# Optimization experiments

Hardware: AMD Instinct MI355X
Metric: run time of the kernel (lower is better)

The kernel has to match this reference:

```python
import jax, jax.numpy as jnp
import numpy as np

TOKENS, IN_F, OUT_F = 8192, 4096, 4096

def setup_inputs() -> dict:
    key = jax.random.key(0)
    k1, k2, k3, k4 = jax.random.split(key, 4)
    # int8 activations and weights in [-127, 127]
    x = jax.random.randint(k1, (TOKENS, IN_F), -127, 128, dtype=jnp.int32).astype(jnp.int8)
    weight = jax.random.randint(k2, (OUT_F, IN_F), -127, 128, dtype=jnp.int32).astype(jnp.int8)  # [out, in]
    # static per-output-channel dequant scale (fp16), small so fp16 output doesn't overflow
    dequant_scale = (jax.random.uniform(k3, (OUT_F,), dtype=jnp.float32) * 1e-3).astype(jnp.float16)
    bias = (jax.random.normal(k4, (OUT_F,), dtype=jnp.float32)).astype(jnp.float16)
    return {"x": x, "weight": weight, "dequant_scale": dequant_scale, "bias": bias}

def reference(x, weight, dequant_scale, bias):
    # int8 GEMM with int32 accumulation: [tokens, in] @ [in, out] -> [tokens, out]
    acc = jax.lax.dot_general(
        x, weight.T,
        dimension_numbers=(((1,), (0,)), ((), ())),
        preferred_element_type=jnp.int32,
    )
    # static per-output-channel dequant, cast to fp16, add fp16 bias
    out = (acc.astype(jnp.float32) * dequant_scale.astype(jnp.float32)[None, :]).astype(jnp.float16)
    out = out + bias[None, :]
    # module returns (output, output_bias)
    return (out, bias)
```

## Files before the change

### kernel.cpp

```cpp
#include <hip/hip_runtime.h>
#include <hip/hip_fp16.h>
#include <stdint.h>

typedef __attribute__((ext_vector_type(4))) int int32x4;
typedef __attribute__((ext_vector_type(4))) float float32x4;

#define TOKENS 8192
#define IN_F   4096
#define OUT_F  4096
#define BM 256
#define BN 256
#define BK 128
#define NT (IN_F / BK)
#define ESTR 260

#define AS1 __attribute__((address_space(1)))
#define AS3 __attribute__((address_space(3)))

__global__ __launch_bounds__(256)
void pack_all_kernel(const int* __restrict__ x32, const int* __restrict__ w32,
                     const float* __restrict__ bias,
                     uint32_t* __restrict__ x8, uint32_t* __restrict__ w8,
                     float* __restrict__ bias_out)
{
    const int gid = blockIdx.x * 256 + threadIdx.x;
    if (gid < OUT_F / 4) {
        float32x4 b4 = __builtin_nontemporal_load((const float32x4*)bias + gid);
        __builtin_nontemporal_store(b4, (float32x4*)bias_out + gid);
    }

    const int nx4 = TOKENS * IN_F / 4;
    const int nw4 = OUT_F * IN_F / 4;
    for (int i = gid; i < nx4 + nw4; i += gridDim.x * 256) {
        const int* s; uint32_t* d; int j;
        if (i < nx4) { s = x32; d = x8; j = i; }
        else         { s = w32; d = w8; j = i - nx4; }
        int32x4 v = __builtin_nontemporal_load((const int32x4*)s + j);
        d[j] = (uint32_t)(v[0] & 0xff) | ((uint32_t)(v[1] & 0xff) << 8) |
               ((uint32_t)(v[2] & 0xff) << 16) | ((uint32_t)v[3] << 24);
    }
}

__global__ __launch_bounds__(512, 2)
void w8a8_gemm_kernel(const int8_t* __restrict__ x,
                      const int8_t* __restrict__ w,
                      const float* __restrict__ scale,
                      const float* __restrict__ bias,
                      float* __restrict__ out)
{
    __shared__ int8_t smem[131072];
    int8_t* lA = smem;
    int8_t* lB = smem + 65536;

    const int tid = threadIdx.x;
    const int wv  = tid >> 6;
    const int l   = tid & 63;
    const int wqm = wv >> 1;
    const int wqn = wv & 1;

    const int xc  = blockIdx.x & 7;
    const int idx = blockIdx.x >> 3;
    const int bn  = (xc & 1) * 8 + (idx & 7);
    const int bm  = (xc >> 1) * 8 + (idx >> 3);

    const int8_t* baseA = x + (size_t)bm * BM * IN_F;
    const int8_t* baseB = w + (size_t)bn * BN * IN_F;

    const int seg0 = wv * 2, seg1 = wv * 2 + 1;
    const int r8   = l >> 3;
    const int swc  = (((l & 7) ^ r8) << 4);

    const int8_t* pA0 = baseA + (size_t)(seg0 * 8 + r8) * IN_F + swc;
    const int8_t* pA1 = baseA + (size_t)(seg1 * 8 + r8) * IN_F + swc;
    const int8_t* pB0 = baseB + (size_t)(seg0 * 8 + r8) * IN_F + swc;
    const int8_t* pB1 = baseB + (size_t)(seg1 * 8 + r8) * IN_F + swc;

    const int fr  = l & 15;
    const int xk  = (l & 7) << 4;
    const int cb0 = (l >> 4) << 4;

    int32x4 acc[2][2][2][4];
#pragma unroll
    for (int a0 = 0; a0 < 2; ++a0)
#pragma unroll
        for (int a1 = 0; a1 < 2; ++a1)
#pragma unroll
            for (int a2 = 0; a2 < 2; ++a2)
#pragma unroll
                for (int a3 = 0; a3 < 4; ++a3)
                    acc[a0][a1][a2][a3] = (int32x4){0, 0, 0, 0};

    int32x4 aF[2][2][2];
    int32x4 bF[2][4][2];

    auto stage_half = [&](int h4) {
        const int kt_ = h4 >> 2;
        const int wh_ = h4 & 3;
        const size_t off = (size_t)(wh_ & 1) * (128 * IN_F) + (size_t)kt_ * BK;
        const int8_t* s0 = ((wh_ < 2) ? pA0 : pB0) + off;
        const int8_t* s1 = ((wh_ < 2) ? pA1 : pB1) + off;
        int8_t* db = ((wh_ < 2) ? lA : lB) + ((kt_ & 1) << 15) + ((wh_ & 1) << 14);
        __builtin_amdgcn_global_load_lds(
            (const AS1 void*)s0, (AS3 void*)(db + seg0 * 1024), 16, 0, 0);
        __builtin_amdgcn_global_load_lds(
            (const AS1 void*)s1, (AS3 void*)(db + seg1 * 1024), 16, 0, 0);
    };

#define LDA(MH)                                                                        \
    do {                                                                               \
        _Pragma("unroll") for (int mi = 0; mi < 2; ++mi)                               \
        _Pragma("unroll") for (int ks = 0; ks < 2; ++ks)                               \
            aF[MH][mi][ks] = *(const int32x4*)&lAb[((MH) << 14) +                      \
                (wqm * 32 + mi * 16 + fr) * 128 + (((ks * 64) + cb0) ^ xk)];           \
    } while (0)

#define LDB(NH)                                                                        \
    do {                                                                               \
        _Pragma("unroll") for (int ni = 0; ni < 4; ++ni)                               \
        _Pragma("unroll") for (int ks = 0; ks < 2; ++ks)                               \
            bF[NH][ni][ks] = *(const int32x4*)&lBb[((NH) << 14) +                      \
                (wqn * 64 + ni * 16 + fr) * 128 + (((ks * 64) + cb0) ^ xk)];           \
    } while (0)

#define MMAQ(MH, NH)                                                                   \
    do {                                                                               \
        _Pragma("unroll") for (int mi = 0; mi < 2; ++mi)                               \
        _Pragma("unroll") for (int ni = 0; ni < 4; ++ni)                               \
        _Pragma("unroll") for (int ks = 0; ks < 2; ++ks)                               \
            acc[MH][NH][mi][ni] = __builtin_amdgcn_mfma_i32_16x16x64_i8(               \
                aF[MH][mi][ks], bF[NH][ni][ks], acc[MH][NH][mi][ni], 0, 0, 0);         \
    } while (0)

    stage_half(0); stage_half(1); stage_half(2); stage_half(3);
    asm volatile("s_waitcnt vmcnt(0)" ::: "memory");
    __builtin_amdgcn_s_barrier();

    for (int t = 0; t < NT; ++t) {
        const int8_t* lAb = lA + ((t & 1) << 15);
        const int8_t* lBb = lB + ((t & 1) << 15);

        LDA(0); LDB(0); LDB(1); LDA(1);

        if (t + 1 < NT) {
            stage_half(4 * (t + 1) + 0); stage_half(4 * (t + 1) + 1);
            stage_half(4 * (t + 1) + 2); stage_half(4 * (t + 1) + 3);
        }

        __builtin_amdgcn_s_setprio(1);
        MMAQ(0, 0); MMAQ(0, 1); MMAQ(1, 0); MMAQ(1, 1);
        __builtin_amdgcn_s_setprio(0);

        if (t + 1 < NT) asm volatile("s_waitcnt vmcnt(0)" ::: "memory");
        __builtin_amdgcn_s_barrier();
    }

    __syncthreads();
    int* eL = (int*)smem;
    const int c4   = tid & 63;
    const int rowt = tid >> 6;
    const float32x4 sc4 = ((const float32x4*)scale)[bn * 64 + c4];
    const float32x4 bf4 = ((const float32x4*)bias )[bn * 64 + c4];
    const __half bh[4] = { __float2half(bf4[0]), __float2half(bf4[1]),
                           __float2half(bf4[2]), __float2half(bf4[3]) };
    const int r0 = (l >> 4) << 2;
    const int wr0 = (wqm & 1) * 32 + r0;

    for (int c = 0; c < 4; ++c) {
        if ((wqm >> 1) == (c & 1)) {
            const int MH = c >> 1;
#pragma unroll
            for (int NH = 0; NH < 2; ++NH)
#pragma unroll
                for (int mi = 0; mi < 2; ++mi)
#pragma unroll
                    for (int ni = 0; ni < 4; ++ni)
#pragma unroll
                        for (int r = 0; r < 4; ++r)
                            eL[(wr0 + mi * 16 + r) * ESTR +
                               NH * 128 + wqn * 64 + ni * 16 + fr] = acc[MH][NH][mi][ni][r];
        }
        __syncthreads();
#pragma unroll
        for (int p = 0; p < 8; ++p) {
            const int rl = p * 8 + rowt;
            int32x4 v = *(const int32x4*)&eL[rl * ESTR + c4 * 4];
            float32x4 o;
#pragma unroll
            for (int j = 0; j < 4; ++j) {
                __half h = __float2half((float)v[j] * sc4[j]);
                o[j] = __half2float(__hadd(h, bh[j]));
            }
            const size_t rowg = (size_t)(bm * 256 + c * 64 + rl);
            __builtin_nontemporal_store(o, (float32x4*)out + rowg * (OUT_F / 4) + bn * 64 + c4);
        }
        __syncthreads();
    }
#undef LDA
#undef LDB
#undef MMAQ
}

extern "C" void kernel_launch(void* const* d_in, const int* in_sizes, int n_in,
                              void* d_out, int out_size, void* d_ws, size_t ws_size,
                              hipStream_t stream)
{
    const int*   x32   = (const int*)d_in[0];
    const int*   w32   = (const int*)d_in[1];
    const float* scale = (const float*)d_in[2];
    const float* bias  = (const float*)d_in[3];
    float* out = (float*)d_out;

    int8_t* x8 = (int8_t*)d_ws;
    int8_t* w8 = x8 + (size_t)TOKENS * IN_F;

    pack_all_kernel<<<3072, 256, 0, stream>>>(x32, w32, bias, (uint32_t*)x8, (uint32_t*)w8,
                                              out + (size_t)TOKENS * OUT_F);

    w8a8_gemm_kernel<<<512, 512, 0, stream>>>(x8, w8, scale, bias, out);
}
```

Baseline: 185.9 us.

## Double-buffer MFMA fragments across K halves and prefetch global tiles two ahead

The main loop now splits each K tile into two 64-wide halves, each with its own register fragment set. LDS reads for one half are issued while the MFMAs of the other half run, and the first half of the next tile is read before the current tile's second-half MFMAs. Global-to-LDS staging is issued for tile t+2 into the buffer just freed, and the prologue preloads two tiles. The goal is to hide LDS read latency behind matrix math. The cost is an extra barrier and lgkmcnt wait per iteration, plus more fragment registers, which may pressure occupancy at 2 waves per SIMD.

```diff
diff --git a/kernel.cpp b/kernel.cpp
--- a/kernel.cpp
+++ b/kernel.cpp
@@ -81,17 +81,17 @@
 
     int32x4 acc[2][2][2][4];
 #pragma unroll
-    for (int a0 = 0; a0 < 2; ++a0)
-#pragma unroll
-        for (int a1 = 0; a1 < 2; ++a1)
-#pragma unroll
-            for (int a2 = 0; a2 < 2; ++a2)
-#pragma unroll
-                for (int a3 = 0; a3 < 4; ++a3)
-                    acc[a0][a1][a2][a3] = (int32x4){0, 0, 0, 0};
-
-    int32x4 aF[2][2][2];
-    int32x4 bF[2][4][2];
+    for (int a0i = 0; a0i < 2; ++a0i)
+#pragma unroll
+        for (int a1i = 0; a1i < 2; ++a1i)
+#pragma unroll
+            for (int a2i = 0; a2i < 2; ++a2i)
+#pragma unroll
+                for (int a3i = 0; a3i < 4; ++a3i)
+                    acc[a0i][a1i][a2i][a3i] = (int32x4){0, 0, 0, 0};
+
+    int32x4 a0[2][2], b0[2][4];
+    int32x4 a1[2][2], b1[2][4];
 
     auto stage_half = [&](int h4) {
         const int kt_ = h4 >> 2;
@@ -105,52 +105,64 @@
         __builtin_amdgcn_global_load_lds(
             (const AS1 void*)s1, (AS3 void*)(db + seg1 * 1024), 16, 0, 0);
     };
-
-#define LDA(MH)                                                                        \
+    auto stage_tile = [&](int tt) {
+        stage_half(4 * tt + 0); stage_half(4 * tt + 1);
+        stage_half(4 * tt + 2); stage_half(4 * tt + 3);
+    };
+
+#define LDFA(DST, LABP, KS)                                                            \
     do {                                                                               \
+        _Pragma("unroll") for (int MH = 0; MH < 2; ++MH)                               \
         _Pragma("unroll") for (int mi = 0; mi < 2; ++mi)                               \
-        _Pragma("unroll") for (int ks = 0; ks < 2; ++ks)                               \
-            aF[MH][mi][ks] = *(const int32x4*)&lAb[((MH) << 14) +                      \
-                (wqm * 32 + mi * 16 + fr) * 128 + (((ks * 64) + cb0) ^ xk)];           \
+            DST[MH][mi] = *(const int32x4*)&(LABP)[(MH << 14) +                        \
+                (wqm * 32 + mi * 16 + fr) * 128 + ((((KS) * 64) + cb0) ^ xk)];         \
     } while (0)
 
-#define LDB(NH)                                                                        \
+#define LDFB(DST, LBBP, KS)                                                            \
     do {                                                                               \
+        _Pragma("unroll") for (int NH = 0; NH < 2; ++NH)                               \
         _Pragma("unroll") for (int ni = 0; ni < 4; ++ni)                               \
-        _Pragma("unroll") for (int ks = 0; ks < 2; ++ks)                               \
-            bF[NH][ni][ks] = *(const int32x4*)&lBb[((NH) << 14) +                      \
-                (wqn * 64 + ni * 16 + fr) * 128 + (((ks * 64) + cb0) ^ xk)];           \
+            DST[NH][ni] = *(const int32x4*)&(LBBP)[(NH << 14) +                        \
+                (wqn * 64 + ni * 16 + fr) * 128 + ((((KS) * 64) + cb0) ^ xk)];         \
     } while (0)
 
-#define MMAQ(MH, NH)                                                                   \
+#define MMA_ALL(AS_, BS_)                                                              \
     do {                                                                               \
+        _Pragma("unroll") for (int MH = 0; MH < 2; ++MH)                               \
+        _Pragma("unroll") for (int NH = 0; NH < 2; ++NH)                               \
         _Pragma("unroll") for (int mi = 0; mi < 2; ++mi)                               \
         _Pragma("unroll") for (int ni = 0; ni < 4; ++ni)                               \
-        _Pragma("unroll") for (int ks = 0; ks < 2; ++ks)                               \
             acc[MH][NH][mi][ni] = __builtin_amdgcn_mfma_i32_16x16x64_i8(               \
-                aF[MH][mi][ks], bF[NH][ni][ks], acc[MH][NH][mi][ni], 0, 0, 0);         \
+                AS_[MH][mi], BS_[NH][ni], acc[MH][NH][mi][ni], 0, 0, 0);               \
     } while (0)
 
-    stage_half(0); stage_half(1); stage_half(2); stage_half(3);
+    stage_tile(0); stage_tile(1);
     asm volatile("s_waitcnt vmcnt(0)" ::: "memory");
     __builtin_amdgcn_s_barrier();
+    LDFA(a0, lA, 0); LDFB(b0, lB, 0);
 
     for (int t = 0; t < NT; ++t) {
-        const int8_t* lAb = lA + ((t & 1) << 15);
-        const int8_t* lBb = lB + ((t & 1) << 15);
-
-        LDA(0); LDB(0); LDB(1); LDA(1);
-
-        if (t + 1 < NT) {
-            stage_half(4 * (t + 1) + 0); stage_half(4 * (t + 1) + 1);
-            stage_half(4 * (t + 1) + 2); stage_half(4 * (t + 1) + 3);
-        }
-
+        const int8_t* curA = lA + ((t & 1) << 15);
+        const int8_t* curB = lB + ((t & 1) << 15);
+        const int8_t* othA = lA + (((t + 1) & 1) << 15);
+        const int8_t* othB = lB + (((t + 1) & 1) << 15);
+
+        LDFA(a1, curA, 1); LDFB(b1, curB, 1);
         __builtin_amdgcn_s_setprio(1);
-        MMAQ(0, 0); MMAQ(0, 1); MMAQ(1, 0); MMAQ(1, 1);
+        MMA_ALL(a0, b0);
         __builtin_amdgcn_s_setprio(0);
-
-        if (t + 1 < NT) asm volatile("s_waitcnt vmcnt(0)" ::: "memory");
+        __builtin_amdgcn_sched_barrier(0);
+        asm volatile("s_waitcnt lgkmcnt(0)" ::: "memory");
+        __builtin_amdgcn_s_barrier();
+
+        if (t + 1 < NT) { LDFA(a0, othA, 0); LDFB(b0, othB, 0); }
+        if (t + 2 < NT) stage_tile(t + 2);
+        __builtin_amdgcn_s_setprio(1);
+        MMA_ALL(a1, b1);
+        __builtin_amdgcn_s_setprio(0);
+        __builtin_amdgcn_sched_barrier(0);
+        asm volatile("s_waitcnt lgkmcnt(0)" ::: "memory");
+        if (t + 2 < NT) asm volatile("s_waitcnt vmcnt(0)" ::: "memory");
         __builtin_amdgcn_s_barrier();
     }
 
@@ -195,9 +207,9 @@
         }
         __syncthreads();
     }
-#undef LDA
-#undef LDB
-#undef MMAQ
+#undef LDFA
+#undef LDFB
+#undef MMA_ALL
 }
 
 extern "C" void kernel_launch(void* const* d_in, const int* in_sizes, int n_in,
```

Measured after the change: 188.0 us. No clear change (+1.1%).

## Remap warps to 128x64 tiles and software-pipeline LDS reads with MFMA phases

Applied to the files above, without the earlier changes.

Each warp now owns 128 rows (4 chunks of 32) by 64 columns instead of the earlier quadrant-split mapping. The k-tile is split into four phases, and each phase issues the LDS reads for the next A chunk while the current chunk's MFMAs run, using double-buffered A and B fragment registers. Global-to-LDS staging is split so that the B half for tile t+2 is issued early, with partial vmcnt and lgkmcnt waits and barriers between phases. The aim is to hide LDS latency and global load latency behind MFMA work, at the cost of more barriers and a fragile hand-tuned wait-count schedule.

```diff
diff --git a/kernel.cpp b/kernel.cpp
--- a/kernel.cpp
+++ b/kernel.cpp
@@ -55,8 +55,10 @@
     const int tid = threadIdx.x;
     const int wv  = tid >> 6;
     const int l   = tid & 63;
-    const int wqm = wv >> 1;
-    const int wqn = wv & 1;
+    const int mgrp = wv >> 2;
+    const int ncol = wv & 3;
+    const int bhalf = ncol >> 1;
+    const int brow  = (ncol & 1) * 64;
 
     const int xc  = blockIdx.x & 7;
     const int idx = blockIdx.x >> 3;
@@ -79,19 +81,17 @@
     const int xk  = (l & 7) << 4;
     const int cb0 = (l >> 4) << 4;
 
-    int32x4 acc[2][2][2][4];
-#pragma unroll
-    for (int a0 = 0; a0 < 2; ++a0)
-#pragma unroll
-        for (int a1 = 0; a1 < 2; ++a1)
-#pragma unroll
-            for (int a2 = 0; a2 < 2; ++a2)
-#pragma unroll
-                for (int a3 = 0; a3 < 4; ++a3)
-                    acc[a0][a1][a2][a3] = (int32x4){0, 0, 0, 0};
-
-    int32x4 aF[2][2][2];
-    int32x4 bF[2][4][2];
+    int32x4 acc[4][2][4];
+#pragma unroll
+    for (int q = 0; q < 4; ++q)
+#pragma unroll
+        for (int mi = 0; mi < 2; ++mi)
+#pragma unroll
+            for (int ni = 0; ni < 4; ++ni)
+                acc[q][mi][ni] = (int32x4){0, 0, 0, 0};
+
+    int32x4 aE[2][2], aO[2][2];
+    int32x4 bS0[4][2], bS1[4][2];
 
     auto stage_half = [&](int h4) {
         const int kt_ = h4 >> 2;
@@ -106,52 +106,80 @@
             (const AS1 void*)s1, (AS3 void*)(db + seg1 * 1024), 16, 0, 0);
     };
 
-#define LDA(MH)                                                                        \
-    do {                                                                               \
+#define LDCH(DST, TT, Q)                                                               \
+    do {                                                                               \
+        const int8_t* _p = lA + (((TT) & 1) << 15) + (mgrp << 14);                     \
         _Pragma("unroll") for (int mi = 0; mi < 2; ++mi)                               \
         _Pragma("unroll") for (int ks = 0; ks < 2; ++ks)                               \
-            aF[MH][mi][ks] = *(const int32x4*)&lAb[((MH) << 14) +                      \
-                (wqm * 32 + mi * 16 + fr) * 128 + (((ks * 64) + cb0) ^ xk)];           \
-    } while (0)
-
-#define LDB(NH)                                                                        \
-    do {                                                                               \
+            DST[mi][ks] = *(const int32x4*)&_p[((Q) * 32 + mi * 16 + fr) * 128 +       \
+                                               (((ks * 64) + cb0) ^ xk)];              \
+    } while (0)
+
+#define LDBO(DST, TT)                                                                  \
+    do {                                                                               \
+        const int8_t* _p = lB + (((TT) & 1) << 15) + (bhalf << 14);                    \
         _Pragma("unroll") for (int ni = 0; ni < 4; ++ni)                               \
         _Pragma("unroll") for (int ks = 0; ks < 2; ++ks)                               \
-            bF[NH][ni][ks] = *(const int32x4*)&lBb[((NH) << 14) +                      \
-                (wqn * 64 + ni * 16 + fr) * 128 + (((ks * 64) + cb0) ^ xk)];           \
-    } while (0)
-
-#define MMAQ(MH, NH)                                                                   \
+            DST[ni][ks] = *(const int32x4*)&_p[(brow + ni * 16 + fr) * 128 +           \
+                                               (((ks * 64) + cb0) ^ xk)];              \
+    } while (0)
+
+#define MMACH(Q, ASET, BSET)                                                           \
     do {                                                                               \
         _Pragma("unroll") for (int mi = 0; mi < 2; ++mi)                               \
         _Pragma("unroll") for (int ni = 0; ni < 4; ++ni)                               \
         _Pragma("unroll") for (int ks = 0; ks < 2; ++ks)                               \
-            acc[MH][NH][mi][ni] = __builtin_amdgcn_mfma_i32_16x16x64_i8(               \
-                aF[MH][mi][ks], bF[NH][ni][ks], acc[MH][NH][mi][ni], 0, 0, 0);         \
+            acc[Q][mi][ni] = __builtin_amdgcn_mfma_i32_16x16x64_i8(                    \
+                ASET[mi][ks], BSET[ni][ks], acc[Q][mi][ni], 0, 0, 0);                  \
+    } while (0)
+
+#define PH_TAIL(Q, ASET, BCUR)                                                         \
+        __builtin_amdgcn_sched_barrier(0);                                             \
+        __builtin_amdgcn_s_setprio(1);                                                 \
+        MMACH(Q, ASET, BCUR);                                                          \
+        __builtin_amdgcn_s_setprio(0);                                                 \
+        __builtin_amdgcn_s_barrier()
+
+#define TILE(T, BCUR, BNXT)                                                            \
+    do {                                                                               \
+                      \
+        LDCH(aO, T, 1);                                                                \
+        if ((T) + 1 < NT) { stage_half(4 * ((T) + 1) + 0);                             \
+                            stage_half(4 * ((T) + 1) + 1); }                           \
+        __builtin_amdgcn_s_barrier();                                                  \
+        asm volatile("s_waitcnt lgkmcnt(4)" ::: "memory");                             \
+        PH_TAIL(0, aE, BCUR);                                                          \
+                                                    \
+        LDCH(aE, T, 2);                                                                \
+        __builtin_amdgcn_s_barrier();                                                  \
+        asm volatile("s_waitcnt lgkmcnt(4)" ::: "memory");                             \
+        PH_TAIL(1, aO, BCUR);                                                          \
+                    \
+        LDCH(aO, T, 3);                                                                \
+        if ((T) + 2 < NT) { stage_half(4 * ((T) + 2) + 2);                             \
+                            stage_half(4 * ((T) + 2) + 3);                             \
+                            asm volatile("s_waitcnt vmcnt(4)" ::: "memory"); }         \
+        else if ((T) + 1 < NT) asm volatile("s_waitcnt vmcnt(0)" ::: "memory");        \
+        __builtin_amdgcn_s_barrier();                                                  \
+        asm volatile("s_waitcnt lgkmcnt(4)" ::: "memory");                             \
+        PH_TAIL(2, aE, BCUR);                                                          \
+                      \
+        if ((T) + 1 < NT) { LDBO(BNXT, (T) + 1); LDCH(aE, (T) + 1, 0); }               \
+        __builtin_amdgcn_s_barrier();                                                  \
+        if ((T) + 1 < NT) asm volatile("s_waitcnt lgkmcnt(12)" ::: "memory");          \
+        else              asm volatile("s_waitcnt lgkmcnt(0)" ::: "memory");           \
+        PH_TAIL(3, aO, BCUR);                                                          \
     } while (0)
 
     stage_half(0); stage_half(1); stage_half(2); stage_half(3);
-    asm volatile("s_waitcnt vmcnt(0)" ::: "memory");
+    stage_half(4 * 1 + 2); stage_half(4 * 1 + 3);
+    asm volatile("s_waitcnt vmcnt(4)" ::: "memory");
     __builtin_amdgcn_s_barrier();
-
-    for (int t = 0; t < NT; ++t) {
-        const int8_t* lAb = lA + ((t & 1) << 15);
-        const int8_t* lBb = lB + ((t & 1) << 15);
-
-        LDA(0); LDB(0); LDB(1); LDA(1);
-
-        if (t + 1 < NT) {
-            stage_half(4 * (t + 1) + 0); stage_half(4 * (t + 1) + 1);
-            stage_half(4 * (t + 1) + 2); stage_half(4 * (t + 1) + 3);
-        }
-
-        __builtin_amdgcn_s_setprio(1);
-        MMAQ(0, 0); MMAQ(0, 1); MMAQ(1, 0); MMAQ(1, 1);
-        __builtin_amdgcn_s_setprio(0);
-
-        if (t + 1 < NT) asm volatile("s_waitcnt vmcnt(0)" ::: "memory");
-        __builtin_amdgcn_s_barrier();
+    LDBO(bS0, 0); LDCH(aE, 0, 0);
+
+    for (int t = 0; t < NT; t += 2) {
+        TILE(t,     bS0, bS1);
+        TILE(t + 1, bS1, bS0);
     }
 
     __syncthreads();
@@ -163,21 +191,20 @@
     const __half bh[4] = { __float2half(bf4[0]), __float2half(bf4[1]),
                            __float2half(bf4[2]), __float2half(bf4[3]) };
     const int r0 = (l >> 4) << 2;
-    const int wr0 = (wqm & 1) * 32 + r0;
 
     for (int c = 0; c < 4; ++c) {
-        if ((wqm >> 1) == (c & 1)) {
-            const int MH = c >> 1;
-#pragma unroll
-            for (int NH = 0; NH < 2; ++NH)
+        if (mgrp == (c >> 1)) {
+            const int Qb = (c & 1) * 2;
+#pragma unroll
+            for (int qq = 0; qq < 2; ++qq)
 #pragma unroll
                 for (int mi = 0; mi < 2; ++mi)
 #pragma unroll
                     for (int ni = 0; ni < 4; ++ni)
 #pragma unroll
                         for (int r = 0; r < 4; ++r)
-                            eL[(wr0 + mi * 16 + r) * ESTR +
-                               NH * 128 + wqn * 64 + ni * 16 + fr] = acc[MH][NH][mi][ni][r];
+                            eL[(qq * 32 + mi * 16 + r0 + r) * ESTR +
+                               ncol * 64 + ni * 16 + fr] = acc[Qb + qq][mi][ni][r];
         }
         __syncthreads();
 #pragma unroll
@@ -195,9 +222,11 @@
         }
         __syncthreads();
     }
-#undef LDA
-#undef LDB
-#undef MMAQ
+#undef LDCH
+#undef LDBO
+#undef MMACH
+#undef PH_TAIL
+#undef TILE
 }
 
 extern "C" void kernel_launch(void* const* d_in, const int* in_sizes, int n_in,
```

Result: slower. 256.4 us (+37.9%).

## Shrink GEMM block tile to 128x128 with 256 threads and 2048 blocks

Applied to the files above, without the earlier changes.

Reworks the int8 GEMM kernel from 256x256 tiles with 8 waves to 128x128 tiles with 4 waves. Each wave now computes a 64x64 sub-tile. The block grid grows to 2048 and LDS per block halves to 64KB, so more blocks can be resident per CU and the work balances better across CUs. The cost is lower arithmetic intensity per block, because each loaded byte feeds fewer MFMAs, which raises global and L2 traffic. The staging, fragment loads and epilogue are rewritten to match the new tile shape.

```diff
diff --git a/kernel.cpp b/kernel.cpp
--- a/kernel.cpp
+++ b/kernel.cpp
@@ -8,11 +8,11 @@
 #define TOKENS 8192
 #define IN_F   4096
 #define OUT_F  4096
-#define BM 256
-#define BN 256
+#define BM 128
+#define BN 128
 #define BK 128
 #define NT (IN_F / BK)
-#define ESTR 260
+#define ESTR 132
 
 #define AS1 __attribute__((address_space(1)))
 #define AS3 __attribute__((address_space(3)))
@@ -41,113 +41,97 @@
     }
 }
 
-__global__ __launch_bounds__(512, 2)
+__global__ __launch_bounds__(256, 2)
 void w8a8_gemm_kernel(const int8_t* __restrict__ x,
                       const int8_t* __restrict__ w,
                       const float* __restrict__ scale,
                       const float* __restrict__ bias,
                       float* __restrict__ out)
 {
-    __shared__ int8_t smem[131072];
+    __shared__ int8_t smem[65536];
     int8_t* lA = smem;
-    int8_t* lB = smem + 65536;
+    int8_t* lB = smem + 32768;
 
     const int tid = threadIdx.x;
     const int wv  = tid >> 6;
     const int l   = tid & 63;
-    const int wqm = wv >> 1;
-    const int wqn = wv & 1;
+    const int wm  = wv >> 1;
+    const int wn  = wv & 1;
 
     const int xc  = blockIdx.x & 7;
     const int idx = blockIdx.x >> 3;
-    const int bn  = (xc & 1) * 8 + (idx & 7);
-    const int bm  = (xc >> 1) * 8 + (idx >> 3);
+    const int bn  = (xc & 1) * 16 + (idx & 15);
+    const int bm  = (xc >> 1) * 16 + (idx >> 4);
 
     const int8_t* baseA = x + (size_t)bm * BM * IN_F;
     const int8_t* baseB = w + (size_t)bn * BN * IN_F;
 
-    const int seg0 = wv * 2, seg1 = wv * 2 + 1;
-    const int r8   = l >> 3;
-    const int swc  = (((l & 7) ^ r8) << 4);
-
-    const int8_t* pA0 = baseA + (size_t)(seg0 * 8 + r8) * IN_F + swc;
-    const int8_t* pA1 = baseA + (size_t)(seg1 * 8 + r8) * IN_F + swc;
-    const int8_t* pB0 = baseB + (size_t)(seg0 * 8 + r8) * IN_F + swc;
-    const int8_t* pB1 = baseB + (size_t)(seg1 * 8 + r8) * IN_F + swc;
+    const int r8  = l >> 3;
+    const int swc = (((l & 7) ^ r8) << 4);
+    const int8_t* pA = baseA + (size_t)(wv * 8 + r8) * IN_F + swc;
+    const int8_t* pB = baseB + (size_t)(wv * 8 + r8) * IN_F + swc;
+    const int dofs = tid << 4;
 
     const int fr  = l & 15;
     const int xk  = (l & 7) << 4;
     const int cb0 = (l >> 4) << 4;
 
-    int32x4 acc[2][2][2][4];
+    int32x4 acc[4][4];
 #pragma unroll
-    for (int a0 = 0; a0 < 2; ++a0)
+    for (int mi = 0; mi < 4; ++mi)
 #pragma unroll
-        for (int a1 = 0; a1 < 2; ++a1)
+        for (int ni = 0; ni < 4; ++ni)
+            acc[mi][ni] = (int32x4){0, 0, 0, 0};
+
+    int32x4 aF[4][2], bF[4][2];
+
+    auto stage_tile = [&](int t) {
+        int8_t* dA = lA + ((t & 1) << 14);
+        int8_t* dB = lB + ((t & 1) << 14);
+        const size_t co = (size_t)t * BK;
 #pragma unroll
-            for (int a2 = 0; a2 < 2; ++a2)
-#pragma unroll
-                for (int a3 = 0; a3 < 4; ++a3)
-                    acc[a0][a1][a2][a3] = (int32x4){0, 0, 0, 0};
-
-    int32x4 aF[2][2][2];
-    int32x4 bF[2][4][2];
-
-    auto stage_half = [&](int h4) {
-        const int kt_ = h4 >> 2;
-        const int wh_ = h4 & 3;
-        const size_t off = (size_t)(wh_ & 1) * (128 * IN_F) + (size_t)kt_ * BK;
-        const int8_t* s0 = ((wh_ < 2) ? pA0 : pB0) + off;
-        const int8_t* s1 = ((wh_ < 2) ? pA1 : pB1) + off;
-        int8_t* db = ((wh_ < 2) ? lA : lB) + ((kt_ & 1) << 15) + ((wh_ & 1) << 14);
-        __builtin_amdgcn_global_load_lds(
-            (const AS1 void*)s0, (AS3 void*)(db + seg0 * 1024), 16, 0, 0);
-        __builtin_amdgcn_global_load_lds(
-            (const AS1 void*)s1, (AS3 void*)(db + seg1 * 1024), 16, 0, 0);
+        for (int i = 0; i < 4; ++i) {
+            __builtin_amdgcn_global_load_lds(
+                (const AS1 void*)(pA + (size_t)(i * 32) * IN_F + co),
+                (AS3 void*)(dA + i * 4096 + dofs), 16, 0, 0);
+            __builtin_amdgcn_global_load_lds(
+                (const AS1 void*)(pB + (size_t)(i * 32) * IN_F + co),
+                (AS3 void*)(dB + i * 4096 + dofs), 16, 0, 0);
+        }
     };
 
-#define LDA(MH)                                                                        \
-    do {                                                                               \
-        _Pragma("unroll") for (int mi = 0; mi < 2; ++mi)                               \
-        _Pragma("unroll") for (int ks = 0; ks < 2; ++ks)                               \
-            aF[MH][mi][ks] = *(const int32x4*)&lAb[((MH) << 14) +                      \
-                (wqm * 32 + mi * 16 + fr) * 128 + (((ks * 64) + cb0) ^ xk)];           \
-    } while (0)
-
-#define LDB(NH)                                                                        \
-    do {                                                                               \
-        _Pragma("unroll") for (int ni = 0; ni < 4; ++ni)                               \
-        _Pragma("unroll") for (int ks = 0; ks < 2; ++ks)                               \
-            bF[NH][ni][ks] = *(const int32x4*)&lBb[((NH) << 14) +                      \
-                (wqn * 64 + ni * 16 + fr) * 128 + (((ks * 64) + cb0) ^ xk)];           \
-    } while (0)
-
-#define MMAQ(MH, NH)                                                                   \
-    do {                                                                               \
-        _Pragma("unroll") for (int mi = 0; mi < 2; ++mi)                               \
-        _Pragma("unroll") for (int ni = 0; ni < 4; ++ni)                               \
-        _Pragma("unroll") for (int ks = 0; ks < 2; ++ks)                               \
-            acc[MH][NH][mi][ni] = __builtin_amdgcn_mfma_i32_16x16x64_i8(               \
-                aF[MH][mi][ks], bF[NH][ni][ks], acc[MH][NH][mi][ni], 0, 0, 0);         \
-    } while (0)
-
-    stage_half(0); stage_half(1); stage_half(2); stage_half(3);
+    stage_tile(0);
     asm volatile("s_waitcnt vmcnt(0)" ::: "memory");
     __builtin_amdgcn_s_barrier();
 
     for (int t = 0; t < NT; ++t) {
-        const int8_t* lAb = lA + ((t & 1) << 15);
-        const int8_t* lBb = lB + ((t & 1) << 15);
+        const int8_t* lAb = lA + ((t & 1) << 14);
+        const int8_t* lBb = lB + ((t & 1) << 14);
 
-        LDA(0); LDB(0); LDB(1); LDA(1);
+#pragma unroll
+        for (int mi = 0; mi < 4; ++mi)
+#pragma unroll
+            for (int ks = 0; ks < 2; ++ks)
+                aF[mi][ks] = *(const int32x4*)&lAb[(wm * 64 + mi * 16 + fr) * 128 +
+                                                   (((ks * 64) + cb0) ^ xk)];
+#pragma unroll
+        for (int ni = 0; ni < 4; ++ni)
+#pragma unroll
+            for (int ks = 0; ks < 2; ++ks)
+                bF[ni][ks] = *(const int32x4*)&lBb[(wn * 64 + ni * 16 + fr) * 128 +
+                                                   (((ks * 64) + cb0) ^ xk)];
 
-        if (t + 1 < NT) {
-            stage_half(4 * (t + 1) + 0); stage_half(4 * (t + 1) + 1);
-            stage_half(4 * (t + 1) + 2); stage_half(4 * (t + 1) + 3);
-        }
+        if (t + 1 < NT) stage_tile(t + 1);
 
         __builtin_amdgcn_s_setprio(1);
-        MMAQ(0, 0); MMAQ(0, 1); MMAQ(1, 0); MMAQ(1, 1);
+#pragma unroll
+        for (int mi = 0; mi < 4; ++mi)
+#pragma unroll
+            for (int ni = 0; ni < 4; ++ni)
+#pragma unroll
+                for (int ks = 0; ks < 2; ++ks)
+                    acc[mi][ni] = __builtin_amdgcn_mfma_i32_16x16x64_i8(
+                        aF[mi][ks], bF[ni][ks], acc[mi][ni], 0, 0, 0);
         __builtin_amdgcn_s_setprio(0);
 
         if (t + 1 < NT) asm volatile("s_waitcnt vmcnt(0)" ::: "memory");
@@ -156,32 +140,30 @@
 
     __syncthreads();
     int* eL = (int*)smem;
-    const int c4   = tid & 63;
-    const int rowt = tid >> 6;
-    const float32x4 sc4 = ((const float32x4*)scale)[bn * 64 + c4];
-    const float32x4 bf4 = ((const float32x4*)bias )[bn * 64 + c4];
+    const int c4   = tid & 31;
+    const int rowt = tid >> 5;
+    const float32x4 sc4 = ((const float32x4*)scale)[bn * 32 + c4];
+    const float32x4 bf4 = ((const float32x4*)bias )[bn * 32 + c4];
     const __half bh[4] = { __float2half(bf4[0]), __float2half(bf4[1]),
                            __float2half(bf4[2]), __float2half(bf4[3]) };
     const int r0 = (l >> 4) << 2;
-    const int wr0 = (wqm & 1) * 32 + r0;
 
     for (int c = 0; c < 4; ++c) {
-        if ((wqm >> 1) == (c & 1)) {
-            const int MH = c >> 1;
+        if (wm == (c >> 1)) {
 #pragma unroll
-            for (int NH = 0; NH < 2; ++NH)
+            for (int mi2 = 0; mi2 < 2; ++mi2) {
+                const int mi = (c & 1) * 2 + mi2;
 #pragma unroll
-                for (int mi = 0; mi < 2; ++mi)
+                for (int ni = 0; ni < 4; ++ni)
 #pragma unroll
-                    for (int ni = 0; ni < 4; ++ni)
-#pragma unroll
-                        for (int r = 0; r < 4; ++r)
-                            eL[(wr0 + mi * 16 + r) * ESTR +
-                               NH * 128 + wqn * 64 + ni * 16 + fr] = acc[MH][NH][mi][ni][r];
+                    for (int r = 0; r < 4; ++r)
+                        eL[(mi2 * 16 + r0 + r) * ESTR +
+                           wn * 64 + ni * 16 + fr] = acc[mi][ni][r];
+            }
         }
         __syncthreads();
 #pragma unroll
-        for (int p = 0; p < 8; ++p) {
+        for (int p = 0; p < 4; ++p) {
             const int rl = p * 8 + rowt;
             int32x4 v = *(const int32x4*)&eL[rl * ESTR + c4 * 4];
             float32x4 o;
@@ -190,14 +172,11 @@
                 __half h = __float2half((float)v[j] * sc4[j]);
                 o[j] = __half2float(__hadd(h, bh[j]));
             }
-            const size_t rowg = (size_t)(bm * 256 + c * 64 + rl);
-            __builtin_nontemporal_store(o, (float32x4*)out + rowg * (OUT_F / 4) + bn * 64 + c4);
+            const size_t rowg = (size_t)(bm * 128 + c * 32 + rl);
+            __builtin_nontemporal_store(o, (float32x4*)out + rowg * (OUT_F / 4) + bn * 32 + c4);
         }
         __syncthreads();
     }
-#undef LDA
-#undef LDB
-#undef MMAQ
 }
 
 extern "C" void kernel_launch(void* const* d_in, const int* in_sizes, int n_in,
@@ -216,5 +195,5 @@
     pack_all_kernel<<<3072, 256, 0, stream>>>(x32, w32, bias, (uint32_t*)x8, (uint32_t*)w8,
                                               out + (size_t)TOKENS * OUT_F);
 
-    w8a8_gemm_kernel<<<512, 512, 0, stream>>>(x8, w8, scale, bias, out);
+    w8a8_gemm_kernel<<<2048, 256, 0, stream>>>(x8, w8, scale, bias, out);
 }
```

After: 197.8 us. 1.06x slower.
